# Optimization experiments

Measured on AMD Instinct MI355X. Metric: run time of the kernel, lower is better.

The kernel has to match this reference:

```python
import jax, jax.numpy as jnp
import numpy as np

B, S, IN_DIM, OUT_DIM = 4, 2048, 1024, 1024
NEG = -9e15

def _xavier(key, shape, gain=1.414):
    fan_in, fan_out = shape[0], shape[1]
    a = gain * np.sqrt(6.0 / (fan_in + fan_out))
    return jax.random.uniform(key, shape, jnp.float32, -a, a)

def setup_inputs() -> dict:
    key = jax.random.key(0)
    ks = jax.random.split(key, 8)
    x = jax.random.normal(ks[0], (B, S, IN_DIM), jnp.float32)
    W_query = _xavier(ks[1], (IN_DIM, OUT_DIM))
    W_key = _xavier(ks[2], (IN_DIM, OUT_DIM))
    W_value = _xavier(ks[3], (IN_DIM, OUT_DIM))
    # torch Linear default init (kaiming-uniform-ish); values don't matter for correctness baseline
    W1 = _xavier(ks[4], (OUT_DIM + IN_DIM, OUT_DIM), gain=1.0)
    b1 = jnp.zeros((OUT_DIM,), jnp.float32)
    W2 = _xavier(ks[5], (OUT_DIM, OUT_DIM), gain=1.0)
    b2 = jnp.zeros((OUT_DIM,), jnp.float32)
    return {"x": x, "W_query": W_query, "W_key": W_key, "W_value": W_value,
            "W1": W1, "b1": b1, "W2": W2, "b2": b2}

def reference(x, W_query, W_key, W_value, W1, b1, W2, b2):
    # QKV projections: [B,S,in] @ [in,out] -> [B,S,out]
    q = jnp.einsum('bsi,io->bso', x, W_query)
    k = jnp.einsum('bsi,io->bso', x, W_key)
    v = jnp.einsum('bsi,io->bso', x, W_value)
    scale = 1.0 / jnp.sqrt(jnp.float32(OUT_DIM))
    e = jnp.einsum('bqd,bkd->bqk', q, k) * scale  # [B,S,S]
    causal = jnp.tril(jnp.ones((S, S), jnp.float32))  # mask > 0 keeps lower triangle
    attn = jnp.where(causal > 0, e, jnp.float32(NEG))
    attn = jax.nn.softmax(attn, axis=2)
    # dropout: eval mode (train=False) -> identity
    out = jnp.einsum('bqk,bkd->bqd', attn, v)  # [B,S,out]
    h = jnp.concatenate([out, x], axis=-1)  # [B,S,out+in]
    h = jax.nn.relu(jnp.einsum('bsf,fo->bso', h, W1) + b1)
    return jnp.einsum('bsf,fo->bso', h, W2) + b2
```

## Files before the change

### kernel.cpp

```cpp
#include <hip/hip_runtime.h>
#include <stdint.h>

typedef __attribute__((ext_vector_type(8))) short short8;
typedef __attribute__((ext_vector_type(4))) float f32x4;

__device__ __forceinline__ unsigned short f32_to_bf16(float f) {
    unsigned int u = __float_as_uint(f);
    u += 0x7FFFu + ((u >> 16) & 1u);
    return (unsigned short)(u >> 16);
}

__device__ __forceinline__ short8 load8_f32_as_bf16(const float* __restrict__ ap) {
    f32x4 f0 = *(const f32x4*)ap;
    f32x4 f1 = *(const f32x4*)(ap + 4);
    union { short8 s; unsigned short u[8]; } cv;
#pragma unroll
    for (int t = 0; t < 4; ++t) {
        cv.u[t]     = f32_to_bf16(f0[t]);
        cv.u[t + 4] = f32_to_bf16(f1[t]);
    }
    return cv.s;
}

__device__ __forceinline__ void gld_lds16(const void* g, void* l) {
    __builtin_amdgcn_global_load_lds(
        (const __attribute__((address_space(1))) unsigned int*)(unsigned long long)(uintptr_t)g,
        (__attribute__((address_space(3))) unsigned int*)(unsigned int)(uintptr_t)l,
        16, 0, 0);
}

template<int AMODE, int EPI, int SWIZ, bool KLIMIT, int MT>
__global__ __launch_bounds__(256, 4)
void gemm128(const unsigned short* __restrict__ A, const unsigned short* __restrict__ A2,
             int lda, int lda2, int ksplit,
             const unsigned short* __restrict__ B, int ldb,
             void* __restrict__ C, int ldc, int K,
             long aStride, long bStride, long cStride,
             const float* __restrict__ bias, long biasStride, float scale,
             void* __restrict__ C2, int ldc2)
{
    int z = blockIdx.z;
    int mblk, nblk;
    if (SWIZ == 1) {
        int lin = blockIdx.y * gridDim.x + blockIdx.x;
        int mchunk = gridDim.y >> 3;
        int xcd = lin & 7, idx = lin >> 3;
        mblk = xcd * mchunk + idx % mchunk;
        nblk = idx / mchunk;
    } else if (SWIZ == 4) {
        mblk = (z & 2) ? ((int)gridDim.y - 1 - (int)blockIdx.y) : blockIdx.y;
        nblk = blockIdx.x;
    } else if (SWIZ == 5) {
        int x = blockIdx.x;
        int a = (int)sqrtf(2.f * (float)x + 1.f);
        if (a > 15) a = 15;
        while (a < 15 && ((a + 1) * (a + 2) / 2) <= x) ++a;
        while (a > 0 && (a * (a + 1) / 2) > x) --a;
        mblk = a;
        nblk = x - a * (a + 1) / 2;
    } else if (SWIZ == 6) {
        int x = blockIdx.x, yy = blockIdx.y;
        if (z < 2) { mblk = x * 8 + (yy & 7); nblk = yy >> 3; }
        else       { nblk = x * 8 + (yy & 7); mblk = yy >> 3; }
    } else {
        mblk = blockIdx.y;
        nblk = blockIdx.x;
    }
    int m0 = mblk * MT;
    int n0 = nblk * 128;

    const unsigned short* Ab;
    const unsigned short* Bb;
    if (SWIZ == 6) {
        if (z < 2) { Ab = A; Bb = B + (size_t)z * bStride; }
        else       { Ab = B + (size_t)2 * bStride; Bb = A; }
    } else {
        Ab = A + (size_t)z * aStride;
        Bb = B + (size_t)z * bStride;
    }

    __shared__ __align__(16) short As[MT * 64];
    __shared__ __align__(16) short Bs[128 * 64];

    int tid  = threadIdx.x;
    int lane = tid & 63, wid = tid >> 6;
    constexpr int MI = MT / 32;
    int wm = (wid & 1) * (MT / 2), wn = (wid >> 1) * 64;
    int fr = lane & 15, fq = lane >> 4;
    int sw0 = ((fq    ) ^ (fr & 7)) * 16;
    int sw1 = ((fq ^ 4) ^ (fr & 7)) * 16;

    int rS = tid >> 3;
    int cS = ((tid & 7) ^ (rS & 7)) * 8;
    char* AsB = (char*)As; char* BsB = (char*)Bs;

    int kend = KLIMIT ? min(K, m0 + MT) : K;

    f32x4 acc[MI][4];
#pragma unroll
    for (int i = 0; i < MI; ++i)
#pragma unroll
    for (int j = 0; j < 4; ++j) acc[i][j] = f32x4{0.f, 0.f, 0.f, 0.f};

    for (int k0 = 0; k0 < kend; k0 += 64) {
        const unsigned short* Asrc = Ab;
        int koff = k0, ldax = lda;
        if (AMODE == 2 && k0 >= ksplit) { Asrc = A2; koff = k0 - ksplit; ldax = lda2; }
        const unsigned short* pa = Asrc + (size_t)(m0 + rS) * ldax + koff + cS;
        const unsigned short* pb = Bb   + (size_t)(n0 + rS) * ldb  + k0   + cS;
#pragma unroll
        for (int t = 0; t < MT / 32; ++t)
            gld_lds16(pa + (size_t)(32 * t) * ldax, AsB + t * 4096 + tid * 16);
#pragma unroll
        for (int t = 0; t < 4; ++t)
            gld_lds16(pb + (size_t)(32 * t) * ldb,  BsB + t * 4096 + tid * 16);
        __syncthreads();

#pragma unroll
        for (int kh = 0; kh < 2; ++kh) {
            int sw = kh ? sw1 : sw0;
            short8 a[MI], b[4];
#pragma unroll
            for (int i = 0; i < MI; ++i)
                a[i] = *(const short8*)(AsB + (wm + i * 16 + fr) * 128 + sw);
#pragma unroll
            for (int j = 0; j < 4; ++j)
                b[j] = *(const short8*)(BsB + (wn + j * 16 + fr) * 128 + sw);
#pragma unroll
            for (int i = 0; i < MI; ++i)
#pragma unroll
            for (int j = 0; j < 4; ++j)
                acc[i][j] = __builtin_amdgcn_mfma_f32_16x16x32_bf16(a[i], b[j], acc[i][j], 0, 0, 0);
        }
        __syncthreads();
    }

    if (EPI == 0) {
        unsigned short* Cz; int ldcz;
        if (SWIZ == 6 && z >= 2) { Cz = (unsigned short*)C2; ldcz = ldc2; }
        else { Cz = (unsigned short*)C + (size_t)z * cStride; ldcz = ldc; }
#pragma unroll
        for (int i = 0; i < MI; ++i)
#pragma unroll
        for (int j = 0; j < 4; ++j)
#pragma unroll
        for (int r = 0; r < 4; ++r) {
            int row = m0 + wm + i * 16 + fq * 4 + r;
            int col = n0 + wn + j * 16 + fr;
            Cz[(size_t)row * ldcz + col] = f32_to_bf16(acc[i][j][r]);
        }
    } else if (EPI == 6) {
        unsigned short* Cz = (unsigned short*)C + (size_t)z * cStride;
        float* rs = const_cast<float*>(bias) + z * biasStride;
#pragma unroll
        for (int i = 0; i < MI; ++i)
#pragma unroll
        for (int r = 0; r < 4; ++r) {
            int row = m0 + wm + i * 16 + fq * 4 + r;
            float s = 0.f;
#pragma unroll
            for (int j = 0; j < 4; ++j) {
                int col = n0 + wn + j * 16 + fr;
                float e = (col <= row) ? __expf(acc[i][j][r] * scale - 16.f) : 0.f;
                s += e;
                Cz[(size_t)row * ldc + col] = f32_to_bf16(e);
            }
            s += __shfl_xor(s, 1);
            s += __shfl_xor(s, 2);
            s += __shfl_xor(s, 4);
            s += __shfl_xor(s, 8);
            if (fr == 0) atomicAdd(&rs[row], s);
        }
    } else if (EPI == 4) {
        unsigned short* Cz = (unsigned short*)C + (size_t)z * cStride;
#pragma unroll
        for (int i = 0; i < MI; ++i)
#pragma unroll
        for (int r = 0; r < 4; ++r) {
            int row = m0 + wm + i * 16 + fq * 4 + r;
            float inv = 1.f / bias[z * biasStride + row];
#pragma unroll
            for (int j = 0; j < 4; ++j) {
                int col = n0 + wn + j * 16 + fr;
                Cz[(size_t)row * ldc + col] = f32_to_bf16(acc[i][j][r] * inv);
            }
        }
    } else {
#pragma unroll
        for (int i = 0; i < MI; ++i)
#pragma unroll
        for (int j = 0; j < 4; ++j)
#pragma unroll
        for (int r = 0; r < 4; ++r) {
            int row = m0 + wm + i * 16 + fq * 4 + r;
            int col = n0 + wn + j * 16 + fr;
            float v = acc[i][j][r];
            if (EPI == 2) {
                v += bias[col];
                v = v > 0.f ? v : 0.f;
                ((unsigned short*)C + (size_t)z * cStride)[(size_t)row * ldc + col] = f32_to_bf16(v);
            } else {
                ((float*)C + (size_t)z * cStride)[(size_t)row * ldc + col] = v + bias[col];
            }
        }
    }
}

__device__ __forceinline__ void transpose_tile32(const float* __restrict__ in,
                                                 unsigned short* __restrict__ out,
                                                 int rows, int cols, int bx, int by, int tid)
{
    __shared__ float t[32][33];
    int tx = tid & 31, ty = tid >> 5;
    int r0 = by * 32, c0 = bx * 32;
#pragma unroll
    for (int i = 0; i < 4; ++i)
        t[ty + i * 8][tx] = in[(size_t)(r0 + ty + i * 8) * cols + c0 + tx];
    __syncthreads();
#pragma unroll
    for (int i = 0; i < 4; ++i)
        out[(size_t)(c0 + ty + i * 8) * rows + r0 + tx] = f32_to_bf16(t[tx][ty + i * 8]);
}

__global__ __launch_bounds__(256)
void prep_kernel(const float* __restrict__ x,
                 const float* __restrict__ Wq, const float* __restrict__ Wk,
                 const float* __restrict__ Wv, const float* __restrict__ W1,
                 const float* __restrict__ W2,
                 unsigned short* __restrict__ xb, unsigned short* __restrict__ WT,
                 unsigned short* __restrict__ W1T, unsigned short* __restrict__ W2T,
                 float* __restrict__ rsum)
{
    int idx = blockIdx.x;
    int tid = threadIdx.x;
    if (idx < 4096) {
        size_t i = ((size_t)idx * 256 + tid) * 8;
        *(short8*)(xb + i) = load8_f32_as_bf16(x + i);
    } else if (idx < 7168) {
        int t = idx - 4096;
        int w = t >> 10; t &= 1023;
        const float* in = w == 0 ? Wq : (w == 1 ? Wk : Wv);
        transpose_tile32(in, WT + (size_t)w * 1024 * 1024, 1024, 1024,
                         t & 31, t >> 5, tid);
    } else if (idx < 9216) {
        int t = idx - 7168;
        transpose_tile32(W1, W1T, 2048, 1024, t & 31, t >> 5, tid);
    } else if (idx < 10240) {
        int t = idx - 9216;
        transpose_tile32(W2, W2T, 1024, 1024, t & 31, t >> 5, tid);
    } else {
        int t = idx - 10240;
        f32x4 zero = {0.f, 0.f, 0.f, 0.f};
        float* p = rsum + ((size_t)t * 256 + tid) * 8;
        *(f32x4*)p = zero;
        *(f32x4*)(p + 4) = zero;
    }
}

extern "C" void kernel_launch(void* const* d_in, const int* in_sizes, int n_in,
                              void* d_out, int out_size, void* d_ws, size_t ws_size,
                              hipStream_t stream)
{
    const float* x  = (const float*)d_in[0];
    const float* Wq = (const float*)d_in[1];
    const float* Wk = (const float*)d_in[2];
    const float* Wv = (const float*)d_in[3];
    const float* W1 = (const float*)d_in[4];
    const float* b1 = (const float*)d_in[5];
    const float* W2 = (const float*)d_in[6];
    const float* b2 = (const float*)d_in[7];
    float* out = (float*)d_out;

    size_t off = 0;
    auto alloc = [&](size_t bytes) {
        char* r = (char*)d_ws + off;
        off += (bytes + 255) & ~(size_t)255;
        return r;
    };
    const size_t TOK = (size_t)8192 * 1024;
    unsigned short* WT   = (unsigned short*)alloc((size_t)3072 * 1024 * 2);
    unsigned short* W1T  = (unsigned short*)alloc((size_t)1024 * 2048 * 2);
    unsigned short* W2T  = (unsigned short*)alloc((size_t)1024 * 1024 * 2);
    unsigned short* xb   = (unsigned short*)alloc(TOK * 2);
    unsigned short* vT   = (unsigned short*)alloc((size_t)1024 * 8192 * 2);
    unsigned short* attn = (unsigned short*)alloc(TOK * 2);
    float*          rsum = (float*)         alloc((size_t)4 * 2048 * 4);
    unsigned short* q    = (unsigned short*)alloc(TOK * 2);
    unsigned short* k    = (unsigned short*)alloc(TOK * 2);
    unsigned short* S    = (unsigned short*)alloc((size_t)4 * 2048 * 2048 * 2);
    unsigned short* h1   = S;

    prep_kernel<<<10244, 256, 0, stream>>>(x, Wq, Wk, Wv, W1, W2, xb, WT, W1T, W2T, rsum);

    gemm128<0, 0, 6, false, 128><<<dim3(8, 64, 3), 256, 0, stream>>>(
        xb, nullptr, 1024, 0, 0, WT, 1024, q, 1024, 1024,
        0, (long)1024 * 1024, (long)TOK, nullptr, 0, 0.f, vT, 8192);

    gemm128<0, 6, 5, false, 128><<<dim3(136, 1, 4), 256, 0, stream>>>(
        q, nullptr, 1024, 0, 0, k, 1024, S, 2048, 1024,
        (long)2048 * 1024, (long)2048 * 1024, (long)2048 * 2048, rsum, 2048, 0.03125f,
        nullptr, 0);
    gemm128<0, 4, 4, true, 128><<<dim3(8, 16, 4), 256, 0, stream>>>(
        S, nullptr, 2048, 0, 0, vT, 8192, attn, 1024, 2048,
        (long)2048 * 2048, (long)2048, (long)2048 * 1024, rsum, 2048, 0.f, nullptr, 0);

    gemm128<2, 2, 1, false, 128><<<dim3(8, 64, 1), 256, 0, stream>>>(
        attn, xb, 1024, 1024, 1024, W1T, 2048, h1, 1024, 2048, 0, 0, 0, b1, 0, 0.f,
        nullptr, 0);
    gemm128<0, 3, 1, false, 128><<<dim3(8, 64, 1), 256, 0, stream>>>(
        h1, nullptr, 1024, 0, 0, W2T, 1024, out, 1024, 1024, 0, 0, 0, b2, 0, 0.f,
        nullptr, 0);
}
```

Measured before the change: 302.8 us.

## Remap attention-GEMM and QK^T blocks across XCDs and widen prep transpose tiles

Adds an XCD-aware block mapping (SWIZ 7) for the P·V GEMM. It assigns each batch to a pair of XCDs and interleaves short and long causal rows so work balances and each XCD's L2 reuses its own batch's S and vT. The triangular QK^T mapping is permuted so consecutive blocks on one XCD cover contiguous tiles. The prep kernel uses 64x64 transpose tiles with float4 loads and 4-wide bf16 stores, and processes four x chunks per block, which cuts the block count. The new mapping assumes the grid is 8x16x4 and that there are 8 XCDs.

```diff
diff --git a/kernel.cpp b/kernel.cpp
--- a/kernel.cpp
+++ b/kernel.cpp
@@ -2,6 +2,7 @@
 #include <stdint.h>
 
 typedef __attribute__((ext_vector_type(8))) short short8;
+typedef __attribute__((ext_vector_type(4))) short short4v;
 typedef __attribute__((ext_vector_type(4))) float f32x4;
 
 __device__ __forceinline__ unsigned short f32_to_bf16(float f) {
@@ -47,11 +48,10 @@
         int xcd = lin & 7, idx = lin >> 3;
         mblk = xcd * mchunk + idx % mchunk;
         nblk = idx / mchunk;
-    } else if (SWIZ == 4) {
-        mblk = (z & 2) ? ((int)gridDim.y - 1 - (int)blockIdx.y) : blockIdx.y;
-        nblk = blockIdx.x;
     } else if (SWIZ == 5) {
         int x = blockIdx.x;
+        int per = (int)gridDim.x >> 3;
+        x = (x & 7) * per + (x >> 3);
         int a = (int)sqrtf(2.f * (float)x + 1.f);
         if (a > 15) a = 15;
         while (a < 15 && ((a + 1) * (a + 2) / 2) <= x) ++a;
@@ -62,6 +62,15 @@
         int x = blockIdx.x, yy = blockIdx.y;
         if (z < 2) { mblk = x * 8 + (yy & 7); nblk = yy >> 3; }
         else       { nblk = x * 8 + (yy & 7); mblk = yy >> 3; }
+    } else if (SWIZ == 7) {
+        int glin = (int)blockIdx.z * 128 + (int)blockIdx.y * 8 + (int)blockIdx.x;
+        int xcd = glin & 7;
+        int s   = glin >> 3;
+        z = xcd >> 1;
+        int h  = xcd & 1;
+        int jm = s & 7;
+        nblk   = s >> 3;
+        mblk   = (jm & 1) ? (15 - h - (jm >> 1) * 2) : ((jm >> 1) * 2 + h);
     } else {
         mblk = blockIdx.y;
         nblk = blockIdx.x;
@@ -206,20 +215,27 @@
     }
 }
 
-__device__ __forceinline__ void transpose_tile32(const float* __restrict__ in,
+__device__ __forceinline__ void transpose_tile64(const float* __restrict__ in,
                                                  unsigned short* __restrict__ out,
                                                  int rows, int cols, int bx, int by, int tid)
 {
-    __shared__ float t[32][33];
-    int tx = tid & 31, ty = tid >> 5;
-    int r0 = by * 32, c0 = bx * 32;
-#pragma unroll
-    for (int i = 0; i < 4; ++i)
-        t[ty + i * 8][tx] = in[(size_t)(r0 + ty + i * 8) * cols + c0 + tx];
+    __shared__ float t[64][65];
+    int tx = tid & 15, ty = tid >> 4;
+    int r0 = by * 64, c0 = bx * 64;
+#pragma unroll
+    for (int i = 0; i < 4; ++i) {
+        f32x4 v = *(const f32x4*)(in + (size_t)(r0 + ty + i * 16) * cols + c0 + tx * 4);
+#pragma unroll
+        for (int j = 0; j < 4; ++j) t[ty + i * 16][tx * 4 + j] = v[j];
+    }
     __syncthreads();
 #pragma unroll
-    for (int i = 0; i < 4; ++i)
-        out[(size_t)(c0 + ty + i * 8) * rows + r0 + tx] = f32_to_bf16(t[tx][ty + i * 8]);
+    for (int i = 0; i < 4; ++i) {
+        union { short4v s; unsigned short u[4]; } o;
+#pragma unroll
+        for (int j = 0; j < 4; ++j) o.u[j] = f32_to_bf16(t[tx * 4 + j][ty + i * 16]);
+        *(short4v*)(out + (size_t)(c0 + ty + i * 16) * rows + r0 + tx * 4) = o.s;
+    }
 }
 
 __global__ __launch_bounds__(256)
@@ -233,23 +249,26 @@
 {
     int idx = blockIdx.x;
     int tid = threadIdx.x;
-    if (idx < 4096) {
-        size_t i = ((size_t)idx * 256 + tid) * 8;
-        *(short8*)(xb + i) = load8_f32_as_bf16(x + i);
-    } else if (idx < 7168) {
-        int t = idx - 4096;
-        int w = t >> 10; t &= 1023;
+    if (idx < 1024) {
+#pragma unroll
+        for (int it = 0; it < 4; ++it) {
+            size_t i = ((size_t)idx * 4 + it) * 2048 + (size_t)tid * 8;
+            *(short8*)(xb + i) = load8_f32_as_bf16(x + i);
+        }
+    } else if (idx < 1792) {
+        int t = idx - 1024;
+        int w = t >> 8; t &= 255;
         const float* in = w == 0 ? Wq : (w == 1 ? Wk : Wv);
-        transpose_tile32(in, WT + (size_t)w * 1024 * 1024, 1024, 1024,
-                         t & 31, t >> 5, tid);
-    } else if (idx < 9216) {
-        int t = idx - 7168;
-        transpose_tile32(W1, W1T, 2048, 1024, t & 31, t >> 5, tid);
-    } else if (idx < 10240) {
-        int t = idx - 9216;
-        transpose_tile32(W2, W2T, 1024, 1024, t & 31, t >> 5, tid);
+        transpose_tile64(in, WT + (size_t)w * 1024 * 1024, 1024, 1024,
+                         t & 15, t >> 4, tid);
+    } else if (idx < 2304) {
+        int t = idx - 1792;
+        transpose_tile64(W1, W1T, 2048, 1024, t & 15, t >> 4, tid);
+    } else if (idx < 2560) {
+        int t = idx - 2304;
+        transpose_tile64(W2, W2T, 1024, 1024, t & 15, t >> 4, tid);
     } else {
-        int t = idx - 10240;
+        int t = idx - 2560;
         f32x4 zero = {0.f, 0.f, 0.f, 0.f};
         float* p = rsum + ((size_t)t * 256 + tid) * 8;
         *(f32x4*)p = zero;
@@ -290,7 +309,7 @@
     unsigned short* S    = (unsigned short*)alloc((size_t)4 * 2048 * 2048 * 2);
     unsigned short* h1   = S;
 
-    prep_kernel<<<10244, 256, 0, stream>>>(x, Wq, Wk, Wv, W1, W2, xb, WT, W1T, W2T, rsum);
+    prep_kernel<<<2564, 256, 0, stream>>>(x, Wq, Wk, Wv, W1, W2, xb, WT, W1T, W2T, rsum);
 
     gemm128<0, 0, 6, false, 128><<<dim3(8, 64, 3), 256, 0, stream>>>(
         xb, nullptr, 1024, 0, 0, WT, 1024, q, 1024, 1024,
@@ -300,7 +319,7 @@
         q, nullptr, 1024, 0, 0, k, 1024, S, 2048, 1024,
         (long)2048 * 1024, (long)2048 * 1024, (long)2048 * 2048, rsum, 2048, 0.03125f,
         nullptr, 0);
-    gemm128<0, 4, 4, true, 128><<<dim3(8, 16, 4), 256, 0, stream>>>(
+    gemm128<0, 4, 7, true, 128><<<dim3(8, 16, 4), 256, 0, stream>>>(
         S, nullptr, 2048, 0, 0, vT, 8192, attn, 1024, 2048,
         (long)2048 * 2048, (long)2048, (long)2048 * 1024, rsum, 2048, 0.f, nullptr, 0);
 
```

New measurement: 289.9 us. -4.2%, faster.
